# Kernel optimization log

Hardware: AMD Instinct MI355X
Metric: run time of the kernel (lower is better)

The kernel has to match this reference:

```python
import jax, jax.numpy as jnp
import numpy as np

B, T, C, H = 2, 2048, 1024, 16
D = C // H  # head dim 64

def setup_inputs() -> dict:
    key = jax.random.key(0)
    k1, k2, k3 = jax.random.split(key, 3)
    x = jax.random.normal(k1, (B, T, C), dtype=jnp.float32)
    W_attn = jax.random.normal(k2, (C, 3 * C), dtype=jnp.float32) * (1.0 / np.sqrt(C))
    b_attn = jnp.zeros((3 * C,), dtype=jnp.float32)
    W_proj = jax.random.normal(k3, (C, C), dtype=jnp.float32) * (1.0 / np.sqrt(C))
    b_proj = jnp.zeros((C,), dtype=jnp.float32)
    return {"x": x, "W_attn": W_attn, "b_attn": b_attn, "W_proj": W_proj, "b_proj": b_proj}

def reference(x, W_attn, b_attn, W_proj, b_proj):
    Bsz, Tlen, Cdim = x.shape
    qkv = x @ W_attn + b_attn  # [B,T,3C]
    q, k, v = jnp.split(qkv, 3, axis=2)
    # [B,T,C] -> [B,H,T,D]
    q = q.reshape(Bsz, Tlen, H, D).transpose(0, 2, 1, 3)
    k = k.reshape(Bsz, Tlen, H, D).transpose(0, 2, 1, 3)
    v = v.reshape(Bsz, Tlen, H, D).transpose(0, 2, 1, 3)
    att = jnp.einsum('bhqd,bhkd->bhqk', q, k) * (1.0 / np.sqrt(D))
    causal = jnp.tril(jnp.ones((Tlen, Tlen), dtype=bool))
    att = jnp.where(causal[None, None, :, :], att, jnp.float32(-jnp.inf))
    att = jax.nn.softmax(att, axis=-1)
    y = jnp.einsum('bhqk,bhkd->bhqd', att, v)  # [B,H,T,D]
    y = y.transpose(0, 2, 1, 3).reshape(Bsz, Tlen, Cdim)
    return y @ W_proj + b_proj
```

## Files before the change

### kernel.cpp

```cpp
#include <hip/hip_runtime.h>
#include <math.h>

#define BSZ 2
#define TSEQ 2048
#define CDIM 1024
#define HNUM 16

typedef __attribute__((ext_vector_type(8))) short bhalf8;
typedef __attribute__((ext_vector_type(4))) short bhalf4;
typedef __attribute__((ext_vector_type(4))) float floatx4;

__device__ __forceinline__ unsigned short f2bf(float f) {
    union { float f; unsigned u; } v;
    v.f = f;
    unsigned r = v.u + 0x7FFFu + ((v.u >> 16) & 1u);
    return (unsigned short)(r >> 16);
}

__device__ __forceinline__ floatx4 fx4_zero() { floatx4 z = {0.f,0.f,0.f,0.f}; return z; }

typedef __attribute__((address_space(3))) unsigned int lds_u32;
typedef const __attribute__((address_space(1))) unsigned int g_u32;
__device__ __forceinline__ void async_copy16(const void* g, void* l) {
    __builtin_amdgcn_global_load_lds((g_u32*)g, (lds_u32*)l, 16, 0, 0);
}

__device__ __forceinline__ void trans_tile(
    const float* __restrict__ W, unsigned short* __restrict__ Wt,
    int K, int N, int n0, int k0, int tid, float (*t)[33])
{
    const int tx = tid & 31, ty = tid >> 5;
#pragma unroll
    for (int i = 0; i < 4; ++i)
        t[ty + i * 8][tx] = W[(size_t)(k0 + ty + i * 8) * N + n0 + tx];
    __syncthreads();
#pragma unroll
    for (int i = 0; i < 4; ++i)
        Wt[(size_t)(n0 + ty + i * 8) * K + k0 + tx] = f2bf(t[tx][ty + i * 8]);
}

__global__ __launch_bounds__(256) void prepass(
    const float* __restrict__ x, unsigned short* __restrict__ xb,
    const float* __restrict__ Wa, unsigned short* __restrict__ WtA,
    const float* __restrict__ Wp, unsigned short* __restrict__ WtP)
{
    __shared__ float t[32][33];
    const int bid = blockIdx.x;
    const int tid = threadIdx.x;
    if (bid < 2048) {
        size_t i = ((size_t)bid * 256 + tid) * 8;
        float4 a = *(const float4*)(x + i);
        float4 b = *(const float4*)(x + i + 4);
        uint4 o;
        o.x = (unsigned)f2bf(a.x) | ((unsigned)f2bf(a.y) << 16);
        o.y = (unsigned)f2bf(a.z) | ((unsigned)f2bf(a.w) << 16);
        o.z = (unsigned)f2bf(b.x) | ((unsigned)f2bf(b.y) << 16);
        o.w = (unsigned)f2bf(b.z) | ((unsigned)f2bf(b.w) << 16);
        *(uint4*)(xb + i) = o;
    } else if (bid < 5120) {
        int tl = bid - 2048;
        trans_tile(Wa, WtA, 1024, 3072, (tl % 96) * 32, (tl / 96) * 32, tid, t);
    } else {
        int tl = bid - 5120;
        trans_tile(Wp, WtP, 1024, 1024, (tl % 32) * 32, (tl / 32) * 32, tid, t);
    }
}

template<int BM, bool OUT_BF16>
__global__ __launch_bounds__(256) void gemm_bt(
    const unsigned short* __restrict__ A, const unsigned short* __restrict__ Bt,
    const float* __restrict__ bias, void* __restrict__ Cp,
    int M, int N, int K, int v_start, unsigned short* __restrict__ vt, int q_end)
{
    constexpr int ALINES = BM / 64;
    constexpr int MT = BM / 32;
    __shared__ unsigned short As[2][BM * 32];
    __shared__ unsigned short Bs[2][128 * 32];

    const int tid   = threadIdx.x;
    const int bm    = blockIdx.y;
    const int bn    = blockIdx.x;
    const int wave  = tid >> 6;
    const int col16 = tid & 15;
    const int quad  = (tid & 63) >> 4;
    const int wm    = (wave >> 1) * (BM / 2);
    const int wn    = (wave & 1) * 64;

    floatx4 acc[MT][4];
#pragma unroll
    for (int i = 0; i < MT; ++i)
#pragma unroll
        for (int j = 0; j < 4; ++j) acc[i][j] = fx4_zero();

    const int gr = tid >> 2;
    const int gk = (tid & 3) * 8;
    const unsigned short* Ab = A  + (size_t)(bm * BM + gr) * K + gk;
    const unsigned short* Bb = Bt + (size_t)(bn * 128 + gr) * K + gk;

#define STAGE(k0, bf) { \
    char* AsB = (char*)As[bf] + wave * 1024; \
    char* BsB = (char*)Bs[bf] + wave * 1024; \
    _Pragma("unroll") \
    for (int l = 0; l < ALINES; ++l) \
        async_copy16(Ab + (size_t)l * 64 * K + (k0), AsB + l * 4096); \
    async_copy16(Bb + (k0), BsB); \
    async_copy16(Bb + (size_t)64 * K + (k0), BsB + 4096); }

#define COMPUTE(bf) { \
    bhalf8 a[MT], b[4]; \
    _Pragma("unroll") \
    for (int i = 0; i < MT; ++i) \
        a[i] = *(const bhalf8*)&As[bf][(wm + i * 16 + col16) * 32 + quad * 8]; \
    _Pragma("unroll") \
    for (int j = 0; j < 4; ++j) \
        b[j] = *(const bhalf8*)&Bs[bf][(wn + j * 16 + col16) * 32 + quad * 8]; \
    _Pragma("unroll") \
    for (int i = 0; i < MT; ++i) \
        _Pragma("unroll") \
        for (int j = 0; j < 4; ++j) \
            acc[i][j] = __builtin_amdgcn_mfma_f32_16x16x32_bf16(a[i], b[j], acc[i][j], 0, 0, 0); }

    STAGE(0, 0);
    __syncthreads();
    int buf = 0;
    for (int k0 = 0; k0 < K - 32; k0 += 32) {
        STAGE(k0 + 32, buf ^ 1);
        COMPUTE(buf);
        __syncthreads();
        buf ^= 1;
    }
    COMPUTE(buf);
#undef STAGE
#undef COMPUTE

    const int colbase = bn * 128 + wn;
    const bool vpath = (v_start >= 0) && (colbase >= v_start);
    const float csc = (colbase < q_end) ? 0.18033688f : 1.0f;
#pragma unroll
    for (int j = 0; j < 4; ++j) {
        int col = colbase + j * 16 + col16;
        float bv = bias[col];
#pragma unroll
        for (int i = 0; i < MT; ++i) {
            if (vpath) {
                int row0 = bm * BM + wm + i * 16 + quad * 4;
                ushort4 o;
                o.x = f2bf((acc[i][j][0] + bv) * csc);
                o.y = f2bf((acc[i][j][1] + bv) * csc);
                o.z = f2bf((acc[i][j][2] + bv) * csc);
                o.w = f2bf((acc[i][j][3] + bv) * csc);
                size_t vrow = (size_t)((row0 >> 11) * 1024 + (col - v_start));
                *(ushort4*)(vt + vrow * 2048 + (row0 & 2047)) = o;
            } else {
#pragma unroll
                for (int r = 0; r < 4; ++r) {
                    int row = bm * BM + wm + i * 16 + quad * 4 + r;
                    float v = (acc[i][j][r] + bv) * csc;
                    if (OUT_BF16)
                        ((unsigned short*)Cp)[(size_t)row * N + col] = f2bf(v);
                    else
                        ((float*)Cp)[(size_t)row * N + col] = v;
                }
            }
        }
    }
}

template<bool DIAG>
__device__ __forceinline__ void attn_tile(
    const unsigned short* __restrict__ Ks, const unsigned short* __restrict__ Vt,
    const bhalf8* qf, floatx4* oT, floatx4& accl,
    int col16, int quad, int qloc)
{
    const int sx = col16 & 7;
    const floatx4 minusC = {-17.31234049f, -17.31234049f, -17.31234049f, -17.31234049f};
    const bhalf4 ones = {0x3F80, 0x3F80, 0x3F80, 0x3F80};

    floatx4 s[4];
#pragma unroll
    for (int n = 0; n < 4; ++n) {
        const int row = 16 * n + col16;
        bhalf8 k0 = *(const bhalf8*)&Ks[row * 64 + ((quad ^ sx) * 8)];
        bhalf8 k1 = *(const bhalf8*)&Ks[row * 64 + (((4 + quad) ^ sx) * 8)];
        floatx4 t = __builtin_amdgcn_mfma_f32_16x16x32_bf16(k0, qf[0], minusC, 0, 0, 0);
        s[n] = __builtin_amdgcn_mfma_f32_16x16x32_bf16(k1, qf[1], t, 0, 0, 0);
    }

    bhalf4 pb[4];
#pragma unroll
    for (int n = 0; n < 4; ++n) {
        unsigned a[4];
#pragma unroll
        for (int r = 0; r < 4; ++r) {
            float p = exp2f(s[n][r]);
            if (DIAG) {
                if (16 * n + quad * 4 + r > qloc) p = 0.f;
            }
            a[r] = __float_as_uint(p) + 0x8000u;
        }
        union { unsigned u[2]; bhalf4 b; } uu;
        uu.u[0] = (a[0] >> 16) | (a[1] & 0xffff0000u);
        uu.u[1] = (a[2] >> 16) | (a[3] & 0xffff0000u);
        pb[n] = uu.b;
        accl = __builtin_amdgcn_mfma_f32_16x16x16bf16_1k(ones, pb[n], accl, 0, 0, 0);
    }

#pragma unroll
    for (int n = 0; n < 4; ++n) {
#pragma unroll
        for (int dt = 0; dt < 4; ++dt) {
            const int d = 16 * dt + col16;
            const bhalf4 av = *(const bhalf4*)&Vt[d * 76 + 16 * n + quad * 4];
            oT[dt] = __builtin_amdgcn_mfma_f32_16x16x16bf16_1k(av, pb[n], oT[dt], 0, 0, 0);
        }
    }
}

__global__ __launch_bounds__(256) void attn_mfma(
    const unsigned short* __restrict__ qkv,
    const unsigned short* __restrict__ vT,
    unsigned short* __restrict__ yout)
{
    __shared__ unsigned short Kbuf[2][64 * 64];
    __shared__ unsigned short Vbuf[2][64 * 76];

    const int tid   = threadIdx.x;
    const int wave  = tid >> 6;
    const int col16 = tid & 15;
    const int quad  = (tid & 63) >> 4;
    const int qb    = (int)gridDim.y - 1 - (int)blockIdx.y;
    const int bh    = blockIdx.x;
    const int b     = bh >> 4;
    const int h     = bh & 15;

    const unsigned short* base  = qkv + (size_t)b * TSEQ * 3072 + h * 64;
    const unsigned short* kbase = base + CDIM;
    const unsigned short* vtb   = vT + (size_t)(b * 1024 + h * 64) * 2048;

    bhalf8 qf[2];
    {
        const unsigned short* qrow =
            base + (size_t)(qb * 64 + wave * 16 + col16) * 3072 + quad * 8;
        qf[0] = *(const bhalf8*)qrow;
        qf[1] = *(const bhalf8*)(qrow + 32);
    }

    const int krow = tid >> 3;
    const int kchk = (tid & 7) ^ (krow & 7);
    const unsigned short* ksrc0 = kbase + (size_t)krow * 3072 + kchk * 8;
    const unsigned short* ksrc1 = kbase + (size_t)(krow + 32) * 3072 + kchk * 8;

    const int vd  = tid >> 3;
    const int vt0 = (tid & 7) * 8;
    const unsigned short* vsrc0 = vtb + (size_t)vd * 2048 + vt0;
    const unsigned short* vsrc1 = vtb + (size_t)(vd + 32) * 2048 + vt0;

#define KSTAGE(kb, bf) { \
    char* Kd = (char*)Kbuf[bf] + wave * 1024; \
    async_copy16(ksrc0 + (size_t)(kb) * 64 * 3072, Kd); \
    async_copy16(ksrc1 + (size_t)(kb) * 64 * 3072, Kd + 4096); }

    floatx4 oT[4];
#pragma unroll
    for (int dt = 0; dt < 4; ++dt) oT[dt] = fx4_zero();
    floatx4 accl = fx4_zero();
    const int qloc = wave * 16 + col16;

    {
        uint4 nv0 = *(const uint4*)vsrc0;
        uint4 nv1 = *(const uint4*)vsrc1;
        KSTAGE(0, 0);
        *(uint4*)&Vbuf[0][vd * 76 + vt0]        = nv0;
        *(uint4*)&Vbuf[0][(vd + 32) * 76 + vt0] = nv1;
    }
    __syncthreads();
    int buf = 0;
    for (int kb = 0; kb < qb; ++kb) {
        uint4 nv0 = *(const uint4*)(vsrc0 + (size_t)(kb + 1) * 64);
        uint4 nv1 = *(const uint4*)(vsrc1 + (size_t)(kb + 1) * 64);
        KSTAGE(kb + 1, buf ^ 1);
        attn_tile<false>(Kbuf[buf], Vbuf[buf], qf, oT, accl, col16, quad, qloc);
        *(uint4*)&Vbuf[buf ^ 1][vd * 76 + vt0]        = nv0;
        *(uint4*)&Vbuf[buf ^ 1][(vd + 32) * 76 + vt0] = nv1;
        __syncthreads();
        buf ^= 1;
    }
    attn_tile<true>(Kbuf[buf], Vbuf[buf], qf, oT, accl, col16, quad, qloc);
#undef KSTAGE

    const float inv = 1.0f / accl[0];
    const size_t row = (size_t)b * TSEQ + (size_t)qb * 64 + wave * 16 + col16;
#pragma unroll
    for (int dt = 0; dt < 4; ++dt) {
        ushort4 o;
        o.x = f2bf(oT[dt][0] * inv);
        o.y = f2bf(oT[dt][1] * inv);
        o.z = f2bf(oT[dt][2] * inv);
        o.w = f2bf(oT[dt][3] * inv);
        *(ushort4*)(yout + row * CDIM + h * 64 + 16 * dt + quad * 4) = o;
    }
}

extern "C" void kernel_launch(void* const* d_in, const int* in_sizes, int n_in,
                              void* d_out, int out_size, void* d_ws, size_t ws_size,
                              hipStream_t stream)
{
    const float* x      = (const float*)d_in[0];
    const float* W_attn = (const float*)d_in[1];
    const float* b_attn = (const float*)d_in[2];
    const float* W_proj = (const float*)d_in[3];
    const float* b_proj = (const float*)d_in[4];
    float* out = (float*)d_out;

    unsigned short* qkv = (unsigned short*)d_ws;
    unsigned short* y   = qkv + (size_t)4096 * 3072;
    unsigned short* xb  = y   + (size_t)4096 * 1024;
    unsigned short* WtA = xb  + (size_t)4096 * 1024;
    unsigned short* WtP = WtA + (size_t)3072 * 1024;
    unsigned short* vT  = WtP + (size_t)1024 * 1024;

    prepass<<<dim3(6144), 256, 0, stream>>>(x, xb, W_attn, WtA, W_proj, WtP);

    gemm_bt<128, true><<<dim3(3072 / 128, 4096 / 128), 256, 0, stream>>>(
        xb, WtA, b_attn, qkv, 4096, 3072, 1024, 2048, vT, 1024);

    attn_mfma<<<dim3(BSZ * HNUM, TSEQ / 64), 256, 0, stream>>>(qkv, vT, y);

    gemm_bt<64, false><<<dim3(1024 / 128, 4096 / 64), 256, 0, stream>>>(
        y, WtP, b_proj, out, 4096, 1024, 1024, -1, nullptr, 0);
}
```

Before: 179.2 us.

## Split attention accumulators, add MFMA priority hints, shrink projection GEMM tile

The attention tile now splits the row-sum and output accumulators into two independent chains, which shortens the serial MFMA dependency. It also wraps the MFMA sections in s_setprio so waves issuing matrix ops get scheduling priority. Separately, the output-projection GEMM becomes templated on BN and runs with 64x64 tiles, doubling its block count for better CU occupancy. The cost is extra accumulator registers in attention and less data reuse per block in the projection GEMM.

```diff
diff --git a/kernel.cpp b/kernel.cpp
--- a/kernel.cpp
+++ b/kernel.cpp
@@ -66,16 +66,18 @@
     }
 }
 
-template<int BM, bool OUT_BF16>
+template<int BM, int BN, bool OUT_BF16>
 __global__ __launch_bounds__(256) void gemm_bt(
     const unsigned short* __restrict__ A, const unsigned short* __restrict__ Bt,
     const float* __restrict__ bias, void* __restrict__ Cp,
     int M, int N, int K, int v_start, unsigned short* __restrict__ vt, int q_end)
 {
     constexpr int ALINES = BM / 64;
+    constexpr int BLINES = BN / 64;
     constexpr int MT = BM / 32;
+    constexpr int NT = BN / 32;
     __shared__ unsigned short As[2][BM * 32];
-    __shared__ unsigned short Bs[2][128 * 32];
+    __shared__ unsigned short Bs[2][BN * 32];
 
     const int tid   = threadIdx.x;
     const int bm    = blockIdx.y;
@@ -84,18 +86,18 @@
     const int col16 = tid & 15;
     const int quad  = (tid & 63) >> 4;
     const int wm    = (wave >> 1) * (BM / 2);
-    const int wn    = (wave & 1) * 64;
-
-    floatx4 acc[MT][4];
+    const int wn    = (wave & 1) * (BN / 2);
+
+    floatx4 acc[MT][NT];
 #pragma unroll
     for (int i = 0; i < MT; ++i)
 #pragma unroll
-        for (int j = 0; j < 4; ++j) acc[i][j] = fx4_zero();
+        for (int j = 0; j < NT; ++j) acc[i][j] = fx4_zero();
 
     const int gr = tid >> 2;
     const int gk = (tid & 3) * 8;
     const unsigned short* Ab = A  + (size_t)(bm * BM + gr) * K + gk;
-    const unsigned short* Bb = Bt + (size_t)(bn * 128 + gr) * K + gk;
+    const unsigned short* Bb = Bt + (size_t)(bn * BN + gr) * K + gk;
 
 #define STAGE(k0, bf) { \
     char* AsB = (char*)As[bf] + wave * 1024; \
@@ -103,21 +105,22 @@
     _Pragma("unroll") \
     for (int l = 0; l < ALINES; ++l) \
         async_copy16(Ab + (size_t)l * 64 * K + (k0), AsB + l * 4096); \
-    async_copy16(Bb + (k0), BsB); \
-    async_copy16(Bb + (size_t)64 * K + (k0), BsB + 4096); }
+    _Pragma("unroll") \
+    for (int l = 0; l < BLINES; ++l) \
+        async_copy16(Bb + (size_t)l * 64 * K + (k0), BsB + l * 4096); }
 
 #define COMPUTE(bf) { \
-    bhalf8 a[MT], b[4]; \
+    bhalf8 a[MT], b[NT]; \
     _Pragma("unroll") \
     for (int i = 0; i < MT; ++i) \
         a[i] = *(const bhalf8*)&As[bf][(wm + i * 16 + col16) * 32 + quad * 8]; \
     _Pragma("unroll") \
-    for (int j = 0; j < 4; ++j) \
+    for (int j = 0; j < NT; ++j) \
         b[j] = *(const bhalf8*)&Bs[bf][(wn + j * 16 + col16) * 32 + quad * 8]; \
     _Pragma("unroll") \
     for (int i = 0; i < MT; ++i) \
         _Pragma("unroll") \
-        for (int j = 0; j < 4; ++j) \
+        for (int j = 0; j < NT; ++j) \
             acc[i][j] = __builtin_amdgcn_mfma_f32_16x16x32_bf16(a[i], b[j], acc[i][j], 0, 0, 0); }
 
     STAGE(0, 0);
@@ -133,11 +136,11 @@
 #undef STAGE
 #undef COMPUTE
 
-    const int colbase = bn * 128 + wn;
+    const int colbase = bn * BN + wn;
     const bool vpath = (v_start >= 0) && (colbase >= v_start);
     const float csc = (colbase < q_end) ? 0.18033688f : 1.0f;
 #pragma unroll
-    for (int j = 0; j < 4; ++j) {
+    for (int j = 0; j < NT; ++j) {
         int col = colbase + j * 16 + col16;
         float bv = bias[col];
 #pragma unroll
@@ -169,7 +172,7 @@
 template<bool DIAG>
 __device__ __forceinline__ void attn_tile(
     const unsigned short* __restrict__ Ks, const unsigned short* __restrict__ Vt,
-    const bhalf8* qf, floatx4* oT, floatx4& accl,
+    const bhalf8* qf, floatx4* oTa, floatx4* oTb, floatx4& accl0, floatx4& accl1,
     int col16, int quad, int qloc)
 {
     const int sx = col16 & 7;
@@ -177,6 +180,7 @@
     const bhalf4 ones = {0x3F80, 0x3F80, 0x3F80, 0x3F80};
 
     floatx4 s[4];
+    __builtin_amdgcn_s_setprio(1);
 #pragma unroll
     for (int n = 0; n < 4; ++n) {
         const int row = 16 * n + col16;
@@ -185,6 +189,7 @@
         floatx4 t = __builtin_amdgcn_mfma_f32_16x16x32_bf16(k0, qf[0], minusC, 0, 0, 0);
         s[n] = __builtin_amdgcn_mfma_f32_16x16x32_bf16(k1, qf[1], t, 0, 0, 0);
     }
+    __builtin_amdgcn_s_setprio(0);
 
     bhalf4 pb[4];
 #pragma unroll
@@ -202,18 +207,27 @@
         uu.u[0] = (a[0] >> 16) | (a[1] & 0xffff0000u);
         uu.u[1] = (a[2] >> 16) | (a[3] & 0xffff0000u);
         pb[n] = uu.b;
-        accl = __builtin_amdgcn_mfma_f32_16x16x16bf16_1k(ones, pb[n], accl, 0, 0, 0);
-    }
-
-#pragma unroll
-    for (int n = 0; n < 4; ++n) {
+    }
+    accl0 = __builtin_amdgcn_mfma_f32_16x16x16bf16_1k(ones, pb[0], accl0, 0, 0, 0);
+    accl1 = __builtin_amdgcn_mfma_f32_16x16x16bf16_1k(ones, pb[1], accl1, 0, 0, 0);
+    accl0 = __builtin_amdgcn_mfma_f32_16x16x16bf16_1k(ones, pb[2], accl0, 0, 0, 0);
+    accl1 = __builtin_amdgcn_mfma_f32_16x16x16bf16_1k(ones, pb[3], accl1, 0, 0, 0);
+
+    __builtin_amdgcn_s_setprio(1);
+#pragma unroll
+    for (int np = 0; np < 2; ++np) {
 #pragma unroll
         for (int dt = 0; dt < 4; ++dt) {
             const int d = 16 * dt + col16;
-            const bhalf4 av = *(const bhalf4*)&Vt[d * 76 + 16 * n + quad * 4];
-            oT[dt] = __builtin_amdgcn_mfma_f32_16x16x16bf16_1k(av, pb[n], oT[dt], 0, 0, 0);
+            const int n0 = 2 * np;
+            const bhalf4 av0 = *(const bhalf4*)&Vt[d * 76 + 16 * n0 + quad * 4];
+            const bhalf4 av1 = *(const bhalf4*)&Vt[d * 76 + 16 * (n0 + 1) + quad * 4];
+            floatx4& o = np ? oTb[dt] : oTa[dt];
+            o = __builtin_amdgcn_mfma_f32_16x16x16bf16_1k(av0, pb[n0], o, 0, 0, 0);
+            o = __builtin_amdgcn_mfma_f32_16x16x16bf16_1k(av1, pb[n0 + 1], o, 0, 0, 0);
         }
     }
+    __builtin_amdgcn_s_setprio(0);
 }
 
 __global__ __launch_bounds__(256) void attn_mfma(
@@ -260,10 +274,10 @@
     async_copy16(ksrc0 + (size_t)(kb) * 64 * 3072, Kd); \
     async_copy16(ksrc1 + (size_t)(kb) * 64 * 3072, Kd + 4096); }
 
-    floatx4 oT[4];
-#pragma unroll
-    for (int dt = 0; dt < 4; ++dt) oT[dt] = fx4_zero();
-    floatx4 accl = fx4_zero();
+    floatx4 oTa[4], oTb[4];
+#pragma unroll
+    for (int dt = 0; dt < 4; ++dt) { oTa[dt] = fx4_zero(); oTb[dt] = fx4_zero(); }
+    floatx4 accl0 = fx4_zero(), accl1 = fx4_zero();
     const int qloc = wave * 16 + col16;
 
     {
@@ -279,24 +293,24 @@
         uint4 nv0 = *(const uint4*)(vsrc0 + (size_t)(kb + 1) * 64);
         uint4 nv1 = *(const uint4*)(vsrc1 + (size_t)(kb + 1) * 64);
         KSTAGE(kb + 1, buf ^ 1);
-        attn_tile<false>(Kbuf[buf], Vbuf[buf], qf, oT, accl, col16, quad, qloc);
+        attn_tile<false>(Kbuf[buf], Vbuf[buf], qf, oTa, oTb, accl0, accl1, col16, quad, qloc);
         *(uint4*)&Vbuf[buf ^ 1][vd * 76 + vt0]        = nv0;
         *(uint4*)&Vbuf[buf ^ 1][(vd + 32) * 76 + vt0] = nv1;
         __syncthreads();
         buf ^= 1;
     }
-    attn_tile<true>(Kbuf[buf], Vbuf[buf], qf, oT, accl, col16, quad, qloc);
+    attn_tile<true>(Kbuf[buf], Vbuf[buf], qf, oTa, oTb, accl0, accl1, col16, quad, qloc);
 #undef KSTAGE
 
-    const float inv = 1.0f / accl[0];
+    const float inv = 1.0f / (accl0[0] + accl1[0]);
     const size_t row = (size_t)b * TSEQ + (size_t)qb * 64 + wave * 16 + col16;
 #pragma unroll
     for (int dt = 0; dt < 4; ++dt) {
         ushort4 o;
-        o.x = f2bf(oT[dt][0] * inv);
-        o.y = f2bf(oT[dt][1] * inv);
-        o.z = f2bf(oT[dt][2] * inv);
-        o.w = f2bf(oT[dt][3] * inv);
+        o.x = f2bf((oTa[dt][0] + oTb[dt][0]) * inv);
+        o.y = f2bf((oTa[dt][1] + oTb[dt][1]) * inv);
+        o.z = f2bf((oTa[dt][2] + oTb[dt][2]) * inv);
+        o.w = f2bf((oTa[dt][3] + oTb[dt][3]) * inv);
         *(ushort4*)(yout + row * CDIM + h * 64 + 16 * dt + quad * 4) = o;
     }
 }
@@ -321,11 +335,11 @@
 
     prepass<<<dim3(6144), 256, 0, stream>>>(x, xb, W_attn, WtA, W_proj, WtP);
 
-    gemm_bt<128, true><<<dim3(3072 / 128, 4096 / 128), 256, 0, stream>>>(
+    gemm_bt<128, 128, true><<<dim3(3072 / 128, 4096 / 128), 256, 0, stream>>>(
         xb, WtA, b_attn, qkv, 4096, 3072, 1024, 2048, vT, 1024);
 
     attn_mfma<<<dim3(BSZ * HNUM, TSEQ / 64), 256, 0, stream>>>(qkv, vT, y);
 
-    gemm_bt<64, false><<<dim3(1024 / 128, 4096 / 64), 256, 0, stream>>>(
+    gemm_bt<64, 64, false><<<dim3(1024 / 64, 4096 / 64), 256, 0, stream>>>(
         y, WtP, b_proj, out, 4096, 1024, 1024, -1, nullptr, 0);
 }
```

After: 181.4 us. About the same (+1.2%).
